# Kernel tuning notes

Measured on AMD Instinct MI355X. Metric: run time of the kernel, lower is better.

## Reference

```python
import jax, jax.numpy as jnp
import numpy as np

B, T, M, P = 512, 64, 256, 256


def setup_inputs() -> dict:
    key = jax.random.key(0)
    ks = jax.random.split(key, 17)
    w = lambda i, shape: (jax.random.normal(ks[i], shape, jnp.float32) * 0.05)
    return {
        "encoded_inputs": jax.random.normal(ks[0], (B, T, M), jnp.float32),
        "y": jax.random.normal(ks[1], (B, T, 1), jnp.float32),
        "tar": jax.random.normal(ks[2], (B, 2), jnp.float32),
        "train": 1,
        "Wd_w": w(3, (M, 2 * P)), "Wd_b": w(4, (M,)),
        "Ud_w": w(5, (M, M)),
        "vd_w": w(6, (1, M)),
        "wt_w": w(7, (1, M + 1)), "wt_b": w(8, (1,)),
        "Wy_w": w(9, (P, P + M)), "Wy_b": w(10, (P,)),
        "vy_w": w(11, (1, P)), "vy_b": w(12, (1,)),
        "Wih": w(13, (4 * P, 1)), "Whh": w(14, (4 * P, P)),
        "bih": w(15, (4 * P,)), "bhh": w(16, (4 * P,)),
    }


def _lstm_cell(x, h, c, Wih, Whh, bih, bhh):
    # torch.nn.LSTMCell gate order: i, f, g, o
    g = x @ Wih.T + h @ Whh.T + (bih + bhh)
    i, f, gg, o = jnp.split(g, 4, axis=1)
    c = jax.nn.sigmoid(f) * c + jax.nn.sigmoid(i) * jnp.tanh(gg)
    h = jax.nn.sigmoid(o) * jnp.tanh(c)
    return h, c


def reference(encoded_inputs, y, tar, train,
              Wd_w, Wd_b, Ud_w, vd_w, wt_w, wt_b,
              Wy_w, Wy_b, vy_w, vy_b, Wih, Whh, bih, bhh):
    Bn = encoded_inputs.shape[0]
    Pn = Whh.shape[1]
    Mn = encoded_inputs.shape[2]
    h0 = jnp.zeros((Bn, Pn), encoded_inputs.dtype)
    c0 = jnp.zeros((Bn, Pn), encoded_inputs.dtype)
    ctx0 = jnp.zeros((Bn, Mn), encoded_inputs.dtype)
    # U_d(encoded_inputs) is loop-invariant
    y1 = jnp.einsum('btm,nm->btn', encoded_inputs, Ud_w)  # (B,T,M)

    def attend(h, s):
        x1 = jnp.concatenate([h, s], axis=1) @ Wd_w.T + Wd_b      # (B,M)
        z1 = jnp.tanh(x1[:, None, :] + y1)                        # (B,T,M)
        l = jnp.einsum('btm,m->bt', z1, vd_w[0])                  # (B,T)
        beta = jax.nn.softmax(l, axis=1)
        return jnp.einsum('bt,btm->bm', beta, encoded_inputs)     # (B,M)

    def step(carry, y_t):
        h, s, _ = carry
        c_t = attend(h, s)
        y_til = jnp.concatenate([c_t, y_t], axis=1) @ wt_w.T + wt_b  # (B,1)
        h, s = _lstm_cell(y_til, h, s, Wih, Whh, bih, bhh)
        return (h, s, c_t), None

    (h, s, c_t), _ = jax.lax.scan(step, (h0, c0, ctx0), jnp.swapaxes(y, 0, 1))

    def head(h):
        return (jnp.concatenate([h, c_t], axis=1) @ Wy_w.T + Wy_b) @ vy_w.T + vy_b

    def extra(h, s, inp):
        y_til = jnp.concatenate([c_t, inp], axis=1) @ wt_w.T + wt_b
        h, s = _lstm_cell(y_til, h, s, Wih, Whh, bih, bhh)
        return h, s, head(h)

    y_Tp1 = head(h)
    if train:
        h, s, y_Tp2 = extra(h, s, tar[:, 0:1])
        h, s, y_Tp3 = extra(h, s, tar[:, 1:2])
    else:
        h, s, y_Tp2 = extra(h, s, y_Tp1)
        h, s, y_Tp3 = extra(h, s, y_Tp2)
    return (y_Tp1, y_Tp2, y_Tp3)
```

## Files before the change

### kernel.cpp

```cpp
#include <hip/hip_runtime.h>


typedef unsigned short u16;
typedef unsigned int u32;
typedef _Float16 half_t;
typedef half_t h2 __attribute__((ext_vector_type(2)));

#define BB 512
#define TT 64
#define MM 256
#define PP 256
#define YS 264
#define ES 68
#define NROW 2
#define NTH 1024

#define WD16_OFF  0
#define WHH16_OFF 131072
#define WY16_OFF  393216
#define WQ_ELEMS  524288
#define WQ_BYTES  (WQ_ELEMS * 2)

struct H8 { h2 p[4]; };

#if defined(__has_builtin)
#if __has_builtin(__builtin_amdgcn_fdot2)
#define FDOT2(a, b, c) __builtin_amdgcn_fdot2((a), (b), (c), false)
#endif
#endif
#ifndef FDOT2
__device__ __forceinline__ float FDOT2(h2 a, h2 b, float c) {
  return c + (float)a[0] * (float)b[0] + (float)a[1] * (float)b[1];
}
#endif

__device__ __forceinline__ float dot8(const H8 w, const H8 a, float acc) {
  acc = FDOT2(w.p[0], a.p[0], acc);
  acc = FDOT2(w.p[1], a.p[1], acc);
  acc = FDOT2(w.p[2], a.p[2], acc);
  acc = FDOT2(w.p[3], a.p[3], acc);
  return acc;
}
__device__ __forceinline__ u16 f2h(float f) {
  union { half_t h; u16 u; } x; x.h = (half_t)f; return x.u;
}
__device__ __forceinline__ float h2f(u16 u) {
  union { u16 u; half_t h; } x; x.u = u; return (float)x.h;
}
__device__ __forceinline__ void unpackH8(const H8 v, float f[8]) {
#pragma unroll
  for (int i = 0; i < 8; ++i) f[i] = (float)v.p[i >> 1][i & 1];
}
__device__ __forceinline__ void ldf8(const float* p, float f[8]) {
  float4 a = *(const float4*)p;
  float4 b = *(const float4*)(p + 4);
  f[0]=a.x; f[1]=a.y; f[2]=a.z; f[3]=a.w;
  f[4]=b.x; f[5]=b.y; f[6]=b.z; f[7]=b.w;
}
__device__ __forceinline__ float tanh_fast(float x) {
  float e = __builtin_amdgcn_exp2f(x * 2.885390081777927f);
  return 1.0f - 2.0f * __builtin_amdgcn_rcpf(1.0f + e);
}
__device__ __forceinline__ float sigmoid_fast(float x) {
  float e = __builtin_amdgcn_exp2f(x * -1.4426950408889634f);
  return __builtin_amdgcn_rcpf(1.0f + e);
}

__global__ __launch_bounds__(256) void prep_kernel(
    const float* __restrict__ Wd, const float* __restrict__ Whh,
    const float* __restrict__ Wy, u16* __restrict__ o) {
  int i = blockIdx.x * 256 + threadIdx.x;
  float v;
  if (i < WHH16_OFF) {
    int ki = i & 7, n = (i >> 3) & 255, kb = i >> 11;
    v = Wd[n * 512 + kb * 8 + ki];
  } else if (i < WY16_OFF) {
    int r = i - WHH16_OFF;
    int ki = r & 7, n = (r >> 3) & 1023, kb = r >> 13;
    v = Whh[n * 256 + kb * 8 + ki];
  } else {
    int r = i - WY16_OFF;
    int ki = r & 7, n = (r >> 3) & 255, kb = r >> 11;
    v = Wy[n * 512 + kb * 8 + ki];
  }
  o[i] = f2h(v);
}

template <int WQ>
__global__ __launch_bounds__(NTH, 4) void scan_kernel(
    const float* __restrict__ E,
    const float* __restrict__ yin,
    const float* __restrict__ tar,
    const int*   __restrict__ train,
    const void*  __restrict__ Wd_q,
    const float* __restrict__ Wd_b,
    const float* __restrict__ Ud_w,
    const float* __restrict__ vd_w,
    const float* __restrict__ wt_w,
    const float* __restrict__ wt_b,
    const void*  __restrict__ Wy_q,
    const float* __restrict__ Wy_b,
    const float* __restrict__ vy_w,
    const float* __restrict__ vy_b,
    const float* __restrict__ Wih,
    const void*  __restrict__ Whh_q,
    const float* __restrict__ bih,
    const float* __restrict__ bhh,
    float* __restrict__ out)
{
  __shared__ __align__(16) u16   y1l[NROW][TT * YS];
  __shared__ __align__(16) u16   e16T[NROW][MM * ES];
  __shared__ __align__(16) u32   hs16[NROW][256];
  __shared__ __align__(16) u32   ctx16p[NROW][128];
  __shared__ __align__(16) float px1[4][MM];
  __shared__ __align__(16) float pg[6][MM];
  __shared__ __align__(16) float pg3[4][MM];
  __shared__ __align__(16) float lpart[NROW][8][TT];
  __shared__ __align__(16) u16   betas16[NROW][TT];
  __shared__ __align__(16) float ysh[NROW][TT];
  __shared__ float red[16];
  __shared__ float sc[NROW];

  const int j   = threadIdx.x;
  const int n   = j & 255;
  const int grp = j >> 8;
  const int wv  = j >> 6;
  const int b0  = blockIdx.x * NROW;

  if (j < 512) ((u32*)hs16)[j] = 0;
  float creg0 = 0.f, creg1 = 0.f;

  const float wih0 = Wih[n],       wih1 = Wih[n + 256];
  const float wih2 = Wih[n + 512], wih3 = Wih[n + 768];
  const float bb0 = bih[n]       + bhh[n];
  const float bb1 = bih[n + 256] + bhh[n + 256];
  const float bb2 = bih[n + 512] + bhh[n + 512];
  const float bb3 = bih[n + 768] + bhh[n + 768];
  const float wtM = wt_w[MM], wtb = wt_b[0];

  if (j < NROW * TT)
    ysh[j >> 6][j & 63] = yin[(size_t)(b0 + (j >> 6)) * TT + (j & 63)];

  {
    const float* __restrict__ Eb0 = E + (size_t)b0 * TT * MM;
    for (int i = j; i < NROW * TT * MM; i += NTH) {
      int r = i >> 14;
      int idx = i & 16383;
      int t = idx >> 8, m = idx & 255;
      e16T[r][m * ES + t] = f2h(Eb0[i]);
    }
  }

  {
    const int rs = grp >> 1, ths = grp & 1;
    const float* __restrict__ Eb = E + (size_t)(b0 + rs) * TT * MM;
    const float* __restrict__ Uj = Ud_w + (size_t)n * MM;
    for (int t0 = ths * 32; t0 < ths * 32 + 32; t0 += 16) {
      float acc[16];
#pragma unroll
      for (int i = 0; i < 16; ++i) acc[i] = 0.f;
      for (int m0 = 0; m0 < MM; m0 += 8) {
        float w[8]; ldf8(Uj + m0, w);
#pragma unroll
        for (int tt = 0; tt < 16; ++tt) {
          float e[8]; ldf8(Eb + (size_t)(t0 + tt) * MM + m0, e);
#pragma unroll
          for (int mm = 0; mm < 8; ++mm) acc[tt] = fmaf(e[mm], w[mm], acc[tt]);
        }
      }
#pragma unroll
      for (int tt = 0; tt < 16; ++tt)
        y1l[rs][(t0 + tt) * YS + n] = f2h(acc[tt]);
    }
  }
  __syncthreads();

  auto gates_apply = [&](int r, float gi, float gf, float gg, float go,
                         float ytil) {
    gi += ytil * wih0 + bb0;
    gf += ytil * wih1 + bb1;
    gg += ytil * wih2 + bb2;
    go += ytil * wih3 + bb3;
    float& cr = r ? creg1 : creg0;
    float c = sigmoid_fast(gf) * cr + sigmoid_fast(gi) * tanh_fast(gg);
    float h = sigmoid_fast(go) * tanh_fast(c);
    cr = c;
    u16* hsu = (u16*)hs16[r];
    hsu[n] = f2h(h);
    hsu[256 + n] = f2h(c);
  };

  auto head_store = [&](int outIdx) {
    float p = 0.f;
    const int rr = grp >> 1, seg = grp & 1;
    const u32* st = seg ? ctx16p[rr] : hs16[rr];
    if (WQ) {
      const u16* pw = (const u16*)Wy_q + ((size_t)(seg * 32) * 256 + n) * 8;
#pragma unroll 2
      for (int kb = 0; kb < 32; ++kb) {
        H8 w = *(const H8*)pw; pw += 2048;
        H8 s = *(const H8*)&st[kb * 4];
        p = dot8(w, s, p);
      }
    } else {
      const float* W = (const float*)Wy_q + (size_t)n * 512 + seg * 256;
#pragma unroll 2
      for (int kb = 0; kb < 32; ++kb) {
        H8 sv = *(const H8*)&st[kb * 4];
        float sf[8]; unpackH8(sv, sf);
        float w[8]; ldf8(W + kb * 8, w);
#pragma unroll
        for (int i = 0; i < 8; ++i) p = fmaf(sf[i], w[i], p);
      }
    }
    if (grp) px1[grp - 1][n] = p;
    __syncthreads();
    if (grp == 0) {
      float q0 = (p + px1[0][n] + Wy_b[n]) * vy_w[n];
      float q1 = (px1[1][n] + px1[2][n] + Wy_b[n]) * vy_w[n];
#pragma unroll
      for (int off = 32; off; off >>= 1) {
        q0 += __shfl_xor(q0, off, 64);
        q1 += __shfl_xor(q1, off, 64);
      }
      if ((j & 63) == 0) { red[wv] = q0; red[8 + wv] = q1; }
    }
    __syncthreads();
    if (j == 0) {
      float o0 = red[0] + red[1] + red[2] + red[3] + vy_b[0];
      float o1 = red[8] + red[9] + red[10] + red[11] + vy_b[0];
      out[(size_t)outIdx * BB + b0] = o0;
      out[(size_t)outIdx * BB + b0 + 1] = o1;
      sc[0] = o0; sc[1] = o1;
    }
    __syncthreads();
  };

  auto mv4 = [&](float& m0, float& m1, float& m2, float& m3, float& m4,
                 float& m5) {
    m0 = m1 = m2 = m3 = m4 = m5 = 0.f;
    if (WQ) {
      const u16* Whh16 = (const u16*)Whh_q;
      if (grp < 2) {
        const int kb0 = grp << 4;
        const u16* pw = Whh16 + ((size_t)kb0 * 1024 + n) * 8;
#pragma unroll 2
        for (int kb2 = 0; kb2 < 16; ++kb2) {
          const int kb = kb0 + kb2;
          H8 h0 = *(const H8*)&hs16[0][kb * 4];
          H8 h1 = *(const H8*)&hs16[1][kb * 4];
          H8 w0 = *(const H8*)pw;
          H8 w1 = *(const H8*)(pw + 2048);
          H8 w2 = *(const H8*)(pw + 4096);
          pw += 8192;
          m0 = dot8(w0, h0, m0); m1 = dot8(w0, h1, m1);
          m2 = dot8(w1, h0, m2); m3 = dot8(w1, h1, m3);
          m4 = dot8(w2, h0, m4); m5 = dot8(w2, h1, m5);
        }
      } else {
        const int half = grp - 2;
        const u16* p3 = Whh16 + ((size_t)(half * 16) * 1024 + 768 + n) * 8;
#pragma unroll 2
        for (int kb2 = 0; kb2 < 16; ++kb2) {
          const int kg = half * 16 + kb2;
          H8 w3 = *(const H8*)p3; p3 += 8192;
          H8 h0 = *(const H8*)&hs16[0][kg * 4];
          H8 h1 = *(const H8*)&hs16[1][kg * 4];
          m0 = dot8(w3, h0, m0); m1 = dot8(w3, h1, m1);
        }
      }
    } else {
      const float* Whf = (const float*)Whh_q;
      if (grp < 2) {
        const int kb0 = grp << 4;
        const float* pw0 = Whf + (size_t)n * 256 + kb0 * 8;
        const float* pw1 = pw0 + 256 * 256;
        const float* pw2 = pw0 + 512 * 256;
#pragma unroll 2
        for (int kb2 = 0; kb2 < 16; ++kb2) {
          const int kb = kb0 + kb2;
          H8 h0v = *(const H8*)&hs16[0][kb * 4];
          H8 h1v = *(const H8*)&hs16[1][kb * 4];
          float hf0[8], hf1[8]; unpackH8(h0v, hf0); unpackH8(h1v, hf1);
          float w0[8], w1[8], w2[8];
          ldf8(pw0 + kb2 * 8, w0);
          ldf8(pw1 + kb2 * 8, w1);
          ldf8(pw2 + kb2 * 8, w2);
#pragma unroll
          for (int i = 0; i < 8; ++i) {
            m0 = fmaf(hf0[i], w0[i], m0); m1 = fmaf(hf1[i], w0[i], m1);
            m2 = fmaf(hf0[i], w1[i], m2); m3 = fmaf(hf1[i], w1[i], m3);
            m4 = fmaf(hf0[i], w2[i], m4); m5 = fmaf(hf1[i], w2[i], m5);
          }
        }
      } else {
        const int half = grp - 2;
        const float* p3f = Whf + ((size_t)(768 + n)) * 256 + half * 128;
#pragma unroll 2
        for (int kb2 = 0; kb2 < 16; ++kb2) {
          const int kg = half * 16 + kb2;
          H8 h0v = *(const H8*)&hs16[0][kg * 4];
          H8 h1v = *(const H8*)&hs16[1][kg * 4];
          float hf0[8], hf1[8]; unpackH8(h0v, hf0); unpackH8(h1v, hf1);
          float w3[8]; ldf8(p3f + kb2 * 8, w3);
#pragma unroll
          for (int i = 0; i < 8; ++i) {
            m0 = fmaf(hf0[i], w3[i], m0); m1 = fmaf(hf1[i], w3[i], m1);
          }
        }
      }
    }
  };

  for (int step = 0; step < TT; ++step) {
    float s0 = 0.f, s1 = 0.f, s2 = 0.f, s3 = 0.f, s4 = 0.f, s5 = 0.f;
    {
      float a0 = 0, a1 = 0, a2 = 0, a3 = 0, a4 = 0, a5 = 0;
      if (WQ) {
        const u16* Whh16 = (const u16*)Whh_q;
        if (grp < 2) {
          const int kb0 = grp << 4;
          const u16* pw = Whh16 + ((size_t)kb0 * 1024 + n) * 8;
#pragma unroll 2
          for (int kb2 = 0; kb2 < 16; ++kb2) {
            const int kb = kb0 + kb2;
            H8 h0 = *(const H8*)&hs16[0][kb * 4];
            H8 h1 = *(const H8*)&hs16[1][kb * 4];
            H8 w0 = *(const H8*)pw;
            H8 w1 = *(const H8*)(pw + 2048);
            H8 w2 = *(const H8*)(pw + 4096);
            pw += 8192;
            a0 = dot8(w0, h0, a0); a1 = dot8(w0, h1, a1);
            a2 = dot8(w1, h0, a2); a3 = dot8(w1, h1, a3);
            a4 = dot8(w2, h0, a4); a5 = dot8(w2, h1, a5);
          }
        } else {
          const int half = grp - 2;
          const u16* pd = (const u16*)Wd_q + ((size_t)(half * 32) * 256 + n) * 8;
          const u16* p3 = Whh16 + ((size_t)(half * 16) * 1024 + 768 + n) * 8;
#pragma unroll 2
          for (int kb2 = 0; kb2 < 16; ++kb2) {
            const int kd = half * 32 + kb2 * 2;
            const int kg = half * 16 + kb2;
            H8 s00 = *(const H8*)&hs16[0][kd * 4];
            H8 s01 = *(const H8*)&hs16[0][kd * 4 + 4];
            H8 s10 = *(const H8*)&hs16[1][kd * 4];
            H8 s11 = *(const H8*)&hs16[1][kd * 4 + 4];
            H8 wd0 = *(const H8*)pd;
            H8 wd1 = *(const H8*)(pd + 2048);
            pd += 4096;
            H8 w3 = *(const H8*)p3; p3 += 8192;
            H8 h0 = *(const H8*)&hs16[0][kg * 4];
            H8 h1 = *(const H8*)&hs16[1][kg * 4];
            a0 = dot8(wd0, s00, a0); a0 = dot8(wd1, s01, a0);
            a1 = dot8(wd0, s10, a1); a1 = dot8(wd1, s11, a1);
            a2 = dot8(w3, h0, a2);   a3 = dot8(w3, h1, a3);
          }
        }
      } else {
        const float* Whf = (const float*)Whh_q;
        if (grp < 2) {
          const int kb0 = grp << 4;
          const float* pw0 = Whf + (size_t)n * 256 + kb0 * 8;
          const float* pw1 = pw0 + 256 * 256;
          const float* pw2 = pw0 + 512 * 256;
#pragma unroll 2
          for (int kb2 = 0; kb2 < 16; ++kb2) {
            const int kb = kb0 + kb2;
            H8 h0v = *(const H8*)&hs16[0][kb * 4];
            H8 h1v = *(const H8*)&hs16[1][kb * 4];
            float hf0[8], hf1[8]; unpackH8(h0v, hf0); unpackH8(h1v, hf1);
            float w0[8], w1[8], w2[8];
            ldf8(pw0 + kb2 * 8, w0);
            ldf8(pw1 + kb2 * 8, w1);
            ldf8(pw2 + kb2 * 8, w2);
#pragma unroll
            for (int i = 0; i < 8; ++i) {
              a0 = fmaf(hf0[i], w0[i], a0); a1 = fmaf(hf1[i], w0[i], a1);
              a2 = fmaf(hf0[i], w1[i], a2); a3 = fmaf(hf1[i], w1[i], a3);
              a4 = fmaf(hf0[i], w2[i], a4); a5 = fmaf(hf1[i], w2[i], a5);
            }
          }
        } else {
          const int half = grp - 2;
          const float* Wdf = (const float*)Wd_q + (size_t)n * 512 + half * 256;
          const float* p3f = Whf + ((size_t)(768 + n)) * 256 + half * 128;
#pragma unroll 2
          for (int kb2 = 0; kb2 < 16; ++kb2) {
            const int kd = half * 32 + kb2 * 2;
            const int kg = half * 16 + kb2;
            H8 s00v = *(const H8*)&hs16[0][kd * 4];
            H8 s01v = *(const H8*)&hs16[0][kd * 4 + 4];
            H8 s10v = *(const H8*)&hs16[1][kd * 4];
            H8 s11v = *(const H8*)&hs16[1][kd * 4 + 4];
            float f00[8], f01[8], f10[8], f11[8];
            unpackH8(s00v, f00); unpackH8(s01v, f01);
            unpackH8(s10v, f10); unpackH8(s11v, f11);
            H8 h0v = *(const H8*)&hs16[0][kg * 4];
            H8 h1v = *(const H8*)&hs16[1][kg * 4];
            float hf0[8], hf1[8]; unpackH8(h0v, hf0); unpackH8(h1v, hf1);
            float wd0[8], wd1[8], w3[8];
            ldf8(Wdf + kb2 * 16, wd0);
            ldf8(Wdf + kb2 * 16 + 8, wd1);
            ldf8(p3f + kb2 * 8, w3);
#pragma unroll
            for (int i = 0; i < 8; ++i) {
              a0 = fmaf(f00[i], wd0[i], a0); a0 = fmaf(f01[i], wd1[i], a0);
              a1 = fmaf(f10[i], wd0[i], a1); a1 = fmaf(f11[i], wd1[i], a1);
              a2 = fmaf(hf0[i], w3[i], a2);  a3 = fmaf(hf1[i], w3[i], a3);
            }
          }
        }
      }
      if (grp == 0) {
        s0 = a0; s1 = a1; s2 = a2; s3 = a3; s4 = a4; s5 = a5;
      } else if (grp == 1) {
        pg[0][n] = a0; pg[1][n] = a1; pg[2][n] = a2;
        pg[3][n] = a3; pg[4][n] = a4; pg[5][n] = a5;
      } else if (grp == 2) {
        float bia = Wd_b[n];
        px1[0][n] = a0 + bia; px1[1][n] = a1 + bia;
        pg3[0][n] = a2; pg3[1][n] = a3;
      } else {
        px1[2][n] = a0; px1[3][n] = a1;
        pg3[2][n] = a2; pg3[3][n] = a3;
      }
    }
    __syncthreads();

    {
      const int r = j >> 9, e8 = (j >> 6) & 7, t = j & 63;
      const u16* __restrict__ yrow = &y1l[r][t * YS + e8 * 32];
      const float* __restrict__ xh = &px1[r][e8 * 32];
      const float* __restrict__ xc = &px1[2 + r][e8 * 32];
      const float* __restrict__ vp = vd_w + e8 * 32;
      float lp = 0.f;
#pragma unroll
      for (int m0 = 0; m0 < 32; m0 += 8) {
        H8 yv = *(const H8*)(yrow + m0);
        float yf[8]; unpackH8(yv, yf);
        float xf[8]; ldf8(xh + m0, xf);
        float xg[8]; ldf8(xc + m0, xg);
        float vf[8]; ldf8(vp + m0, vf);
#pragma unroll
        for (int mm = 0; mm < 8; ++mm) {
          float z = tanh_fast(xf[mm] + xg[mm] + yf[mm]);
          lp = fmaf(z, vf[mm], lp);
        }
      }
      lpart[r][e8][t] = lp;
    }
    __syncthreads();

    if ((j & 511) < 64) {
      const int r = j >> 9, t = j & 63;
      float l = lpart[r][0][t] + lpart[r][1][t] + lpart[r][2][t] +
                lpart[r][3][t] + lpart[r][4][t] + lpart[r][5][t] +
                lpart[r][6][t] + lpart[r][7][t];
      float mx = l;
#pragma unroll
      for (int off = 32; off; off >>= 1) mx = fmaxf(mx, __shfl_xor(mx, off, 64));
      float e = __builtin_amdgcn_exp2f((l - mx) * 1.4426950408889634f);
      float sm = e;
#pragma unroll
      for (int off = 32; off; off >>= 1) sm += __shfl_xor(sm, off, 64);
      betas16[r][t] = f2h(e * __builtin_amdgcn_rcpf(sm));
    }
    __syncthreads();

    if (((j >> 8) & 1) == 0) {
      const int r = j >> 9;
      const u16* __restrict__ ep = &e16T[r][n * ES];
      float acc = 0.f;
#pragma unroll
      for (int t0 = 0; t0 < TT; t0 += 8) {
        h2 e0 = *(const h2*)(ep + t0);
        h2 e1 = *(const h2*)(ep + t0 + 2);
        h2 e2 = *(const h2*)(ep + t0 + 4);
        h2 e3 = *(const h2*)(ep + t0 + 6);
        H8 bp = *(const H8*)&betas16[r][t0];
        acc = FDOT2(bp.p[0], e0, acc);
        acc = FDOT2(bp.p[1], e1, acc);
        acc = FDOT2(bp.p[2], e2, acc);
        acc = FDOT2(bp.p[3], e3, acc);
      }
      ((u16*)ctx16p[r])[n] = f2h(acc);
      float p = acc * wt_w[n];
#pragma unroll
      for (int off = 32; off; off >>= 1) p += __shfl_xor(p, off, 64);
      if ((j & 63) == 0) red[wv] = p;
    }
    __syncthreads();

    if (grp == 0) {
      float yt0 = red[0] + red[1] + red[2] + red[3] + ysh[0][step] * wtM + wtb;
      float yt1 = red[8] + red[9] + red[10] + red[11] + ysh[1][step] * wtM + wtb;
      gates_apply(0, s0 + pg[0][n], s2 + pg[2][n], s4 + pg[4][n],
                  pg3[0][n] + pg3[2][n], yt0);
      gates_apply(1, s1 + pg[1][n], s3 + pg[3][n], s5 + pg[5][n],
                  pg3[1][n] + pg3[3][n], yt1);
    }
    __syncthreads();
  }

  if (((j >> 8) & 1) == 0) {
    const int r = j >> 9;
    float p = h2f(((const u16*)ctx16p[r])[n]) * wt_w[n];
#pragma unroll
    for (int off = 32; off; off >>= 1) p += __shfl_xor(p, off, 64);
    if ((j & 63) == 0) red[wv] = p;
  }
  __syncthreads();
  const float ctd0 = red[0] + red[1] + red[2] + red[3];
  const float ctd1 = red[8] + red[9] + red[10] + red[11];

  head_store(0);

  const int tr = train[0];
  for (int e = 0; e < 2; ++e) {
    float m0, m1, m2, m3, m4, m5;
    mv4(m0, m1, m2, m3, m4, m5);
    if (grp == 1) {
      pg[0][n] = m0; pg[1][n] = m1; pg[2][n] = m2;
      pg[3][n] = m3; pg[4][n] = m4; pg[5][n] = m5;
    } else if (grp == 2) {
      pg3[0][n] = m0; pg3[1][n] = m1;
    } else if (grp == 3) {
      pg3[2][n] = m0; pg3[3][n] = m1;
    }
    __syncthreads();
    if (grp == 0) {
      float inp0 = tr ? tar[(size_t)b0 * 2 + e] : sc[0];
      float inp1 = tr ? tar[(size_t)(b0 + 1) * 2 + e] : sc[1];
      float yt0 = ctd0 + inp0 * wtM + wtb;
      float yt1 = ctd1 + inp1 * wtM + wtb;
      gates_apply(0, m0 + pg[0][n], m2 + pg[2][n], m4 + pg[4][n],
                  pg3[0][n] + pg3[2][n], yt0);
      gates_apply(1, m1 + pg[1][n], m3 + pg[3][n], m5 + pg[5][n],
                  pg3[1][n] + pg3[3][n], yt1);
    }
    __syncthreads();
    head_store(1 + e);
  }
}

extern "C" void kernel_launch(void* const* d_in, const int* in_sizes, int n_in,
                              void* d_out, int out_size, void* d_ws, size_t ws_size,
                              hipStream_t stream) {
  const float* E     = (const float*)d_in[0];
  const float* yin   = (const float*)d_in[1];
  const float* tar   = (const float*)d_in[2];
  const int*   train = (const int*)d_in[3];
  const float* Wd_w  = (const float*)d_in[4];
  const float* Wd_b  = (const float*)d_in[5];
  const float* Ud_w  = (const float*)d_in[6];
  const float* vd_w  = (const float*)d_in[7];
  const float* wt_w  = (const float*)d_in[8];
  const float* wt_b  = (const float*)d_in[9];
  const float* Wy_w  = (const float*)d_in[10];
  const float* Wy_b  = (const float*)d_in[11];
  const float* vy_w  = (const float*)d_in[12];
  const float* vy_b  = (const float*)d_in[13];
  const float* Wih   = (const float*)d_in[14];
  const float* Whh   = (const float*)d_in[15];
  const float* bih   = (const float*)d_in[16];
  const float* bhh   = (const float*)d_in[17];

  float* out = (float*)d_out;

  if (ws_size >= (size_t)WQ_BYTES) {
    u16* wq = (u16*)d_ws;
    prep_kernel<<<dim3(WQ_ELEMS / 256), dim3(256), 0, stream>>>(
        Wd_w, Whh, Wy_w, wq);
    scan_kernel<1><<<dim3(BB / NROW), dim3(NTH), 0, stream>>>(
        E, yin, tar, train, wq + WD16_OFF, Wd_b, Ud_w, vd_w, wt_w, wt_b,
        wq + WY16_OFF, Wy_b, vy_w, vy_b, Wih, wq + WHH16_OFF, bih, bhh, out);
  } else {
    scan_kernel<0><<<dim3(BB / NROW), dim3(NTH), 0, stream>>>(
        E, yin, tar, train, Wd_w, Wd_b, Ud_w, vd_w, wt_w, wt_b,
        Wy_w, Wy_b, vy_w, vy_b, Wih, Whh, bih, bhh, out);
  }

  (void)in_sizes; (void)n_in; (void)out_size;
}
```

Before: 1.087 ms.

## Rebalance per-step matvecs evenly across all four thread groups with contiguous weight layout

Repacks the fp16 Wd and Whh weights so each of the 1024 threads reads one contiguous 384-element slice. Every thread now computes an equal share: a quarter-K slice of the Wd projection plus two Whh gate partial sums. This replaces the old scheme where groups did unequal work with strided weight reads. Gate partials are stored as fp16 in shared memory and summed by the gate threads. The softmax and context stages are merged to drop one barrier, and the head matvec gives two rows to each of 512 threads. The fp16 rounding of gate partials adds precision risk, and the tanh input now sums four partial vectors.

```diff
diff --git a/kernel.cpp b/kernel.cpp
--- a/kernel.cpp
+++ b/kernel.cpp
@@ -9,14 +9,11 @@
 #define BB 512
 #define TT 64
 #define MM 256
-#define PP 256
 #define YS 264
 #define ES 68
 #define NROW 2
 #define NTH 1024
 
-#define WD16_OFF  0
-#define WHH16_OFF 131072
 #define WY16_OFF  393216
 #define WQ_ELEMS  524288
 #define WQ_BYTES  (WQ_ELEMS * 2)
@@ -69,21 +66,25 @@
 __global__ __launch_bounds__(256) void prep_kernel(
     const float* __restrict__ Wd, const float* __restrict__ Whh,
     const float* __restrict__ Wy, u16* __restrict__ o) {
-  int i = blockIdx.x * 256 + threadIdx.x;
+  int u = blockIdx.x * 256 + threadIdx.x;
   float v;
-  if (i < WHH16_OFF) {
-    int ki = i & 7, n = (i >> 3) & 255, kb = i >> 11;
-    v = Wd[n * 512 + kb * 8 + ki];
-  } else if (i < WY16_OFF) {
-    int r = i - WHH16_OFF;
-    int ki = r & 7, n = (r >> 3) & 1023, kb = r >> 13;
-    v = Whh[n * 256 + kb * 8 + ki];
+  if (u < WY16_OFF) {
+    int c = u / 384, s = u % 384;
+    int q = c >> 8, n = c & 255;
+    int part = s >> 7, rem = s & 127;
+    if (part == 0) {
+      v = Wd[n * 512 + q * 128 + rem];
+    } else {
+      int g = 2 * (q >> 1) + (part - 1);
+      v = Whh[(n + 256 * g) * 256 + (q & 1) * 128 + rem];
+    }
   } else {
-    int r = i - WY16_OFF;
-    int ki = r & 7, n = (r >> 3) & 255, kb = r >> 11;
-    v = Wy[n * 512 + kb * 8 + ki];
-  }
-  o[i] = f2h(v);
+    int w = u - WY16_OFF;
+    int c = w >> 8, rem = w & 255;
+    int kh = c >> 8, n = c & 255;
+    v = Wy[n * 512 + kh * 256 + rem];
+  }
+  o[u] = f2h(v);
 }
 
 template <int WQ>
@@ -112,18 +113,17 @@
   __shared__ __align__(16) u16   e16T[NROW][MM * ES];
   __shared__ __align__(16) u32   hs16[NROW][256];
   __shared__ __align__(16) u32   ctx16p[NROW][128];
-  __shared__ __align__(16) float px1[4][MM];
-  __shared__ __align__(16) float pg[6][MM];
-  __shared__ __align__(16) float pg3[4][MM];
+  __shared__ __align__(16) float px1[8 * MM];
+  __shared__ __align__(16) u16   pgs[16 * MM];
   __shared__ __align__(16) float lpart[NROW][8][TT];
-  __shared__ __align__(16) u16   betas16[NROW][TT];
+  __shared__ __align__(16) u16   betas16[8][TT];
   __shared__ __align__(16) float ysh[NROW][TT];
   __shared__ float red[16];
   __shared__ float sc[NROW];
 
   const int j   = threadIdx.x;
   const int n   = j & 255;
-  const int grp = j >> 8;
+  const int q   = j >> 8;
   const int wv  = j >> 6;
   const int b0  = blockIdx.x * NROW;
 
@@ -152,7 +152,7 @@
   }
 
   {
-    const int rs = grp >> 1, ths = grp & 1;
+    const int rs = q >> 1, ths = q & 1;
     const float* __restrict__ Eb = E + (size_t)(b0 + rs) * TT * MM;
     const float* __restrict__ Uj = Ud_w + (size_t)n * MM;
     for (int t0 = ths * 32; t0 < ths * 32 + 32; t0 += 16) {
@@ -190,45 +190,62 @@
     hsu[256 + n] = f2h(c);
   };
 
+  auto gate_combine = [&](int r, float& gi, float& gf, float& gg, float& go) {
+    gi = h2f(pgs[(0 * 2 + r) * 256 + n]) + h2f(pgs[(2 * 2 + r) * 256 + n]);
+    gf = h2f(pgs[(1 * 2 + r) * 256 + n]) + h2f(pgs[(3 * 2 + r) * 256 + n]);
+    gg = h2f(pgs[(4 * 2 + r) * 256 + n]) + h2f(pgs[(6 * 2 + r) * 256 + n]);
+    go = h2f(pgs[(5 * 2 + r) * 256 + n]) + h2f(pgs[(7 * 2 + r) * 256 + n]);
+  };
+
   auto head_store = [&](int outIdx) {
-    float p = 0.f;
-    const int rr = grp >> 1, seg = grp & 1;
-    const u32* st = seg ? ctx16p[rr] : hs16[rr];
-    if (WQ) {
-      const u16* pw = (const u16*)Wy_q + ((size_t)(seg * 32) * 256 + n) * 8;
+    if (j < 512) {
+      const int kh = j >> 8, nn = j & 255;
+      float p0 = 0.f, p1 = 0.f;
+      const u32* s0 = kh ? ctx16p[0] : hs16[0];
+      const u32* s1 = kh ? ctx16p[1] : hs16[1];
+      if (WQ) {
+        const u16* pw = (const u16*)Wy_q + ((size_t)(kh * 256 + nn)) * 256;
+#pragma unroll 4
+        for (int i = 0; i < 32; ++i) {
+          H8 w = *(const H8*)(pw + i * 8);
+          H8 a0 = *(const H8*)&s0[i * 4];
+          H8 a1 = *(const H8*)&s1[i * 4];
+          p0 = dot8(w, a0, p0);
+          p1 = dot8(w, a1, p1);
+        }
+      } else {
+        const float* W = (const float*)Wy_q + (size_t)nn * 512 + kh * 256;
 #pragma unroll 2
-      for (int kb = 0; kb < 32; ++kb) {
-        H8 w = *(const H8*)pw; pw += 2048;
-        H8 s = *(const H8*)&st[kb * 4];
-        p = dot8(w, s, p);
-      }
-    } else {
-      const float* W = (const float*)Wy_q + (size_t)n * 512 + seg * 256;
-#pragma unroll 2
-      for (int kb = 0; kb < 32; ++kb) {
-        H8 sv = *(const H8*)&st[kb * 4];
-        float sf[8]; unpackH8(sv, sf);
-        float w[8]; ldf8(W + kb * 8, w);
-#pragma unroll
-        for (int i = 0; i < 8; ++i) p = fmaf(sf[i], w[i], p);
-      }
-    }
-    if (grp) px1[grp - 1][n] = p;
-    __syncthreads();
-    if (grp == 0) {
-      float q0 = (p + px1[0][n] + Wy_b[n]) * vy_w[n];
-      float q1 = (px1[1][n] + px1[2][n] + Wy_b[n]) * vy_w[n];
+        for (int i = 0; i < 32; ++i) {
+          H8 a0v = *(const H8*)&s0[i * 4];
+          H8 a1v = *(const H8*)&s1[i * 4];
+          float a0[8], a1[8]; unpackH8(a0v, a0); unpackH8(a1v, a1);
+          float w[8]; ldf8(W + i * 8, w);
+#pragma unroll
+          for (int m = 0; m < 8; ++m) {
+            p0 = fmaf(a0[m], w[m], p0);
+            p1 = fmaf(a1[m], w[m], p1);
+          }
+        }
+      }
+      px1[(kh * 2 + 0) * 256 + nn] = p0;
+      px1[(kh * 2 + 1) * 256 + nn] = p1;
+    }
+    __syncthreads();
+    if (j < 256) {
+      float q0 = (px1[n] + px1[2 * 256 + n] + Wy_b[n]) * vy_w[n];
+      float q1 = (px1[1 * 256 + n] + px1[3 * 256 + n] + Wy_b[n]) * vy_w[n];
 #pragma unroll
       for (int off = 32; off; off >>= 1) {
         q0 += __shfl_xor(q0, off, 64);
         q1 += __shfl_xor(q1, off, 64);
       }
-      if ((j & 63) == 0) { red[wv] = q0; red[8 + wv] = q1; }
+      if ((j & 63) == 0) { red[wv] = q0; red[4 + wv] = q1; }
     }
     __syncthreads();
     if (j == 0) {
       float o0 = red[0] + red[1] + red[2] + red[3] + vy_b[0];
-      float o1 = red[8] + red[9] + red[10] + red[11] + vy_b[0];
+      float o1 = red[4] + red[5] + red[6] + red[7] + vy_b[0];
       out[(size_t)outIdx * BB + b0] = o0;
       out[(size_t)outIdx * BB + b0 + 1] = o1;
       sc[0] = o0; sc[1] = o1;
@@ -236,215 +253,85 @@
     __syncthreads();
   };
 
-  auto mv4 = [&](float& m0, float& m1, float& m2, float& m3, float& m4,
-                 float& m5) {
-    m0 = m1 = m2 = m3 = m4 = m5 = 0.f;
-    if (WQ) {
-      const u16* Whh16 = (const u16*)Whh_q;
-      if (grp < 2) {
-        const int kb0 = grp << 4;
-        const u16* pw = Whh16 + ((size_t)kb0 * 1024 + n) * 8;
+  const int cw = q * 64;
+  const int gw = (q & 1) * 64;
+
+  for (int step = 0; step < TT; ++step) {
+    {
+      float ax0 = 0.f, ax1 = 0.f;
+      float ga0 = 0.f, ga1 = 0.f, gb0 = 0.f, gb1 = 0.f;
+      if (WQ) {
+        const u16* base = (const u16*)Wd_q + (size_t)j * 384;
+        const u32* h0p = hs16[0];
+        const u32* h1p = hs16[1];
+#pragma unroll 4
+        for (int i = 0; i < 16; ++i) {
+          H8 wd = *(const H8*)(base + i * 8);
+          H8 wa = *(const H8*)(base + 128 + i * 8);
+          H8 wb = *(const H8*)(base + 256 + i * 8);
+          H8 cs0 = *(const H8*)&h0p[cw + i * 4];
+          H8 cs1 = *(const H8*)&h1p[cw + i * 4];
+          H8 hh0 = *(const H8*)&h0p[gw + i * 4];
+          H8 hh1 = *(const H8*)&h1p[gw + i * 4];
+          ax0 = dot8(wd, cs0, ax0); ax1 = dot8(wd, cs1, ax1);
+          ga0 = dot8(wa, hh0, ga0); ga1 = dot8(wa, hh1, ga1);
+          gb0 = dot8(wb, hh0, gb0); gb1 = dot8(wb, hh1, gb1);
+        }
+      } else {
+        const int gsel = 2 * (q >> 1);
+        const float* pwd = (const float*)Wd_q + (size_t)n * 512 + q * 128;
+        const float* pwa = (const float*)Whh_q +
+                           ((size_t)(n + 256 * gsel)) * 256 + (q & 1) * 128;
+        const float* pwb = pwa + 256 * 256;
 #pragma unroll 2
-        for (int kb2 = 0; kb2 < 16; ++kb2) {
-          const int kb = kb0 + kb2;
-          H8 h0 = *(const H8*)&hs16[0][kb * 4];
-          H8 h1 = *(const H8*)&hs16[1][kb * 4];
-          H8 w0 = *(const H8*)pw;
-          H8 w1 = *(const H8*)(pw + 2048);
-          H8 w2 = *(const H8*)(pw + 4096);
-          pw += 8192;
-          m0 = dot8(w0, h0, m0); m1 = dot8(w0, h1, m1);
-          m2 = dot8(w1, h0, m2); m3 = dot8(w1, h1, m3);
-          m4 = dot8(w2, h0, m4); m5 = dot8(w2, h1, m5);
-        }
-      } else {
-        const int half = grp - 2;
-        const u16* p3 = Whh16 + ((size_t)(half * 16) * 1024 + 768 + n) * 8;
-#pragma unroll 2
-        for (int kb2 = 0; kb2 < 16; ++kb2) {
-          const int kg = half * 16 + kb2;
-          H8 w3 = *(const H8*)p3; p3 += 8192;
-          H8 h0 = *(const H8*)&hs16[0][kg * 4];
-          H8 h1 = *(const H8*)&hs16[1][kg * 4];
-          m0 = dot8(w3, h0, m0); m1 = dot8(w3, h1, m1);
-        }
-      }
-    } else {
-      const float* Whf = (const float*)Whh_q;
-      if (grp < 2) {
-        const int kb0 = grp << 4;
-        const float* pw0 = Whf + (size_t)n * 256 + kb0 * 8;
-        const float* pw1 = pw0 + 256 * 256;
-        const float* pw2 = pw0 + 512 * 256;
-#pragma unroll 2
-        for (int kb2 = 0; kb2 < 16; ++kb2) {
-          const int kb = kb0 + kb2;
-          H8 h0v = *(const H8*)&hs16[0][kb * 4];
-          H8 h1v = *(const H8*)&hs16[1][kb * 4];
-          float hf0[8], hf1[8]; unpackH8(h0v, hf0); unpackH8(h1v, hf1);
-          float w0[8], w1[8], w2[8];
-          ldf8(pw0 + kb2 * 8, w0);
-          ldf8(pw1 + kb2 * 8, w1);
-          ldf8(pw2 + kb2 * 8, w2);
-#pragma unroll
-          for (int i = 0; i < 8; ++i) {
-            m0 = fmaf(hf0[i], w0[i], m0); m1 = fmaf(hf1[i], w0[i], m1);
-            m2 = fmaf(hf0[i], w1[i], m2); m3 = fmaf(hf1[i], w1[i], m3);
-            m4 = fmaf(hf0[i], w2[i], m4); m5 = fmaf(hf1[i], w2[i], m5);
+        for (int i = 0; i < 16; ++i) {
+          H8 cs0v = *(const H8*)&hs16[0][cw + i * 4];
+          H8 cs1v = *(const H8*)&hs16[1][cw + i * 4];
+          H8 hh0v = *(const H8*)&hs16[0][gw + i * 4];
+          H8 hh1v = *(const H8*)&hs16[1][gw + i * 4];
+          float c0[8], c1[8], h0f[8], h1f[8];
+          unpackH8(cs0v, c0); unpackH8(cs1v, c1);
+          unpackH8(hh0v, h0f); unpackH8(hh1v, h1f);
+          float wd8[8], wa8[8], wb8[8];
+          ldf8(pwd + i * 8, wd8); ldf8(pwa + i * 8, wa8); ldf8(pwb + i * 8, wb8);
+#pragma unroll
+          for (int m = 0; m < 8; ++m) {
+            ax0 = fmaf(c0[m], wd8[m], ax0); ax1 = fmaf(c1[m], wd8[m], ax1);
+            ga0 = fmaf(h0f[m], wa8[m], ga0); ga1 = fmaf(h1f[m], wa8[m], ga1);
+            gb0 = fmaf(h0f[m], wb8[m], gb0); gb1 = fmaf(h1f[m], wb8[m], gb1);
           }
         }
-      } else {
-        const int half = grp - 2;
-        const float* p3f = Whf + ((size_t)(768 + n)) * 256 + half * 128;
-#pragma unroll 2
-        for (int kb2 = 0; kb2 < 16; ++kb2) {
-          const int kg = half * 16 + kb2;
-          H8 h0v = *(const H8*)&hs16[0][kg * 4];
-          H8 h1v = *(const H8*)&hs16[1][kg * 4];
-          float hf0[8], hf1[8]; unpackH8(h0v, hf0); unpackH8(h1v, hf1);
-          float w3[8]; ldf8(p3f + kb2 * 8, w3);
-#pragma unroll
-          for (int i = 0; i < 8; ++i) {
-            m0 = fmaf(hf0[i], w3[i], m0); m1 = fmaf(hf1[i], w3[i], m1);
-          }
-        }
-      }
-    }
-  };
-
-  for (int step = 0; step < TT; ++step) {
-    float s0 = 0.f, s1 = 0.f, s2 = 0.f, s3 = 0.f, s4 = 0.f, s5 = 0.f;
-    {
-      float a0 = 0, a1 = 0, a2 = 0, a3 = 0, a4 = 0, a5 = 0;
-      if (WQ) {
-        const u16* Whh16 = (const u16*)Whh_q;
-        if (grp < 2) {
-          const int kb0 = grp << 4;
-          const u16* pw = Whh16 + ((size_t)kb0 * 1024 + n) * 8;
-#pragma unroll 2
-          for (int kb2 = 0; kb2 < 16; ++kb2) {
-            const int kb = kb0 + kb2;
-            H8 h0 = *(const H8*)&hs16[0][kb * 4];
-            H8 h1 = *(const H8*)&hs16[1][kb * 4];
-            H8 w0 = *(const H8*)pw;
-            H8 w1 = *(const H8*)(pw + 2048);
-            H8 w2 = *(const H8*)(pw + 4096);
-            pw += 8192;
-            a0 = dot8(w0, h0, a0); a1 = dot8(w0, h1, a1);
-            a2 = dot8(w1, h0, a2); a3 = dot8(w1, h1, a3);
-            a4 = dot8(w2, h0, a4); a5 = dot8(w2, h1, a5);
-          }
-        } else {
-          const int half = grp - 2;
-          const u16* pd = (const u16*)Wd_q + ((size_t)(half * 32) * 256 + n) * 8;
-          const u16* p3 = Whh16 + ((size_t)(half * 16) * 1024 + 768 + n) * 8;
-#pragma unroll 2
-          for (int kb2 = 0; kb2 < 16; ++kb2) {
-            const int kd = half * 32 + kb2 * 2;
-            const int kg = half * 16 + kb2;
-            H8 s00 = *(const H8*)&hs16[0][kd * 4];
-            H8 s01 = *(const H8*)&hs16[0][kd * 4 + 4];
-            H8 s10 = *(const H8*)&hs16[1][kd * 4];
-            H8 s11 = *(const H8*)&hs16[1][kd * 4 + 4];
-            H8 wd0 = *(const H8*)pd;
-            H8 wd1 = *(const H8*)(pd + 2048);
-            pd += 4096;
-            H8 w3 = *(const H8*)p3; p3 += 8192;
-            H8 h0 = *(const H8*)&hs16[0][kg * 4];
-            H8 h1 = *(const H8*)&hs16[1][kg * 4];
-            a0 = dot8(wd0, s00, a0); a0 = dot8(wd1, s01, a0);
-            a1 = dot8(wd0, s10, a1); a1 = dot8(wd1, s11, a1);
-            a2 = dot8(w3, h0, a2);   a3 = dot8(w3, h1, a3);
-          }
-        }
-      } else {
-        const float* Whf = (const float*)Whh_q;
-        if (grp < 2) {
-          const int kb0 = grp << 4;
-          const float* pw0 = Whf + (size_t)n * 256 + kb0 * 8;
-          const float* pw1 = pw0 + 256 * 256;
-          const float* pw2 = pw0 + 512 * 256;
-#pragma unroll 2
-          for (int kb2 = 0; kb2 < 16; ++kb2) {
-            const int kb = kb0 + kb2;
-            H8 h0v = *(const H8*)&hs16[0][kb * 4];
-            H8 h1v = *(const H8*)&hs16[1][kb * 4];
-            float hf0[8], hf1[8]; unpackH8(h0v, hf0); unpackH8(h1v, hf1);
-            float w0[8], w1[8], w2[8];
-            ldf8(pw0 + kb2 * 8, w0);
-            ldf8(pw1 + kb2 * 8, w1);
-            ldf8(pw2 + kb2 * 8, w2);
-#pragma unroll
-            for (int i = 0; i < 8; ++i) {
-              a0 = fmaf(hf0[i], w0[i], a0); a1 = fmaf(hf1[i], w0[i], a1);
-              a2 = fmaf(hf0[i], w1[i], a2); a3 = fmaf(hf1[i], w1[i], a3);
-              a4 = fmaf(hf0[i], w2[i], a4); a5 = fmaf(hf1[i], w2[i], a5);
-            }
-          }
-        } else {
-          const int half = grp - 2;
-          const float* Wdf = (const float*)Wd_q + (size_t)n * 512 + half * 256;
-          const float* p3f = Whf + ((size_t)(768 + n)) * 256 + half * 128;
-#pragma unroll 2
-          for (int kb2 = 0; kb2 < 16; ++kb2) {
-            const int kd = half * 32 + kb2 * 2;
-            const int kg = half * 16 + kb2;
-            H8 s00v = *(const H8*)&hs16[0][kd * 4];
-            H8 s01v = *(const H8*)&hs16[0][kd * 4 + 4];
-            H8 s10v = *(const H8*)&hs16[1][kd * 4];
-            H8 s11v = *(const H8*)&hs16[1][kd * 4 + 4];
-            float f00[8], f01[8], f10[8], f11[8];
-            unpackH8(s00v, f00); unpackH8(s01v, f01);
-            unpackH8(s10v, f10); unpackH8(s11v, f11);
-            H8 h0v = *(const H8*)&hs16[0][kg * 4];
-            H8 h1v = *(const H8*)&hs16[1][kg * 4];
-            float hf0[8], hf1[8]; unpackH8(h0v, hf0); unpackH8(h1v, hf1);
-            float wd0[8], wd1[8], w3[8];
-            ldf8(Wdf + kb2 * 16, wd0);
-            ldf8(Wdf + kb2 * 16 + 8, wd1);
-            ldf8(p3f + kb2 * 8, w3);
-#pragma unroll
-            for (int i = 0; i < 8; ++i) {
-              a0 = fmaf(f00[i], wd0[i], a0); a0 = fmaf(f01[i], wd1[i], a0);
-              a1 = fmaf(f10[i], wd0[i], a1); a1 = fmaf(f11[i], wd1[i], a1);
-              a2 = fmaf(hf0[i], w3[i], a2);  a3 = fmaf(hf1[i], w3[i], a3);
-            }
-          }
-        }
-      }
-      if (grp == 0) {
-        s0 = a0; s1 = a1; s2 = a2; s3 = a3; s4 = a4; s5 = a5;
-      } else if (grp == 1) {
-        pg[0][n] = a0; pg[1][n] = a1; pg[2][n] = a2;
-        pg[3][n] = a3; pg[4][n] = a4; pg[5][n] = a5;
-      } else if (grp == 2) {
-        float bia = Wd_b[n];
-        px1[0][n] = a0 + bia; px1[1][n] = a1 + bia;
-        pg3[0][n] = a2; pg3[1][n] = a3;
-      } else {
-        px1[2][n] = a0; px1[3][n] = a1;
-        pg3[2][n] = a2; pg3[3][n] = a3;
-      }
+      }
+      if (q == 0) { float b = Wd_b[n]; ax0 += b; ax1 += b; }
+      px1[(0 * 4 + q) * 256 + n] = ax0;
+      px1[(1 * 4 + q) * 256 + n] = ax1;
+      pgs[((q * 2 + 0) * 2 + 0) * 256 + n] = f2h(ga0);
+      pgs[((q * 2 + 0) * 2 + 1) * 256 + n] = f2h(ga1);
+      pgs[((q * 2 + 1) * 2 + 0) * 256 + n] = f2h(gb0);
+      pgs[((q * 2 + 1) * 2 + 1) * 256 + n] = f2h(gb1);
     }
     __syncthreads();
 
     {
       const int r = j >> 9, e8 = (j >> 6) & 7, t = j & 63;
-      const u16* __restrict__ yrow = &y1l[r][t * YS + e8 * 32];
-      const float* __restrict__ xh = &px1[r][e8 * 32];
-      const float* __restrict__ xc = &px1[2 + r][e8 * 32];
-      const float* __restrict__ vp = vd_w + e8 * 32;
+      const int mb = e8 * 32;
+      const u16* __restrict__ yrow = &y1l[r][t * YS + mb];
+      const float* p0 = &px1[(r * 4 + 0) * 256 + mb];
+      const float* p1 = &px1[(r * 4 + 1) * 256 + mb];
+      const float* p2 = &px1[(r * 4 + 2) * 256 + mb];
+      const float* p3 = &px1[(r * 4 + 3) * 256 + mb];
+      const float* vp = vd_w + mb;
       float lp = 0.f;
 #pragma unroll
       for (int m0 = 0; m0 < 32; m0 += 8) {
-        H8 yv = *(const H8*)(yrow + m0);
-        float yf[8]; unpackH8(yv, yf);
-        float xf[8]; ldf8(xh + m0, xf);
-        float xg[8]; ldf8(xc + m0, xg);
-        float vf[8]; ldf8(vp + m0, vf);
+        float xa[8], xb[8], xc[8], xd[8], vf[8], yf[8];
+        ldf8(p0 + m0, xa); ldf8(p1 + m0, xb);
+        ldf8(p2 + m0, xc); ldf8(p3 + m0, xd);
+        H8 yv = *(const H8*)(yrow + m0); unpackH8(yv, yf);
+        ldf8(vp + m0, vf);
 #pragma unroll
         for (int mm = 0; mm < 8; ++mm) {
-          float z = tanh_fast(xf[mm] + xg[mm] + yf[mm]);
+          float z = tanh_fast(xa[mm] + xb[mm] + xc[mm] + xd[mm] + yf[mm]);
           lp = fmaf(z, vf[mm], lp);
         }
       }
@@ -452,11 +339,11 @@
     }
     __syncthreads();
 
-    if ((j & 511) < 64) {
-      const int r = j >> 9, t = j & 63;
-      float l = lpart[r][0][t] + lpart[r][1][t] + lpart[r][2][t] +
-                lpart[r][3][t] + lpart[r][4][t] + lpart[r][5][t] +
-                lpart[r][6][t] + lpart[r][7][t];
+    if (j < 512) {
+      const int r = j >> 8, lane = j & 63;
+      float l = lpart[r][0][lane] + lpart[r][1][lane] + lpart[r][2][lane] +
+                lpart[r][3][lane] + lpart[r][4][lane] + lpart[r][5][lane] +
+                lpart[r][6][lane] + lpart[r][7][lane];
       float mx = l;
 #pragma unroll
       for (int off = 32; off; off >>= 1) mx = fmaxf(mx, __shfl_xor(mx, off, 64));
@@ -464,25 +351,22 @@
       float sm = e;
 #pragma unroll
       for (int off = 32; off; off >>= 1) sm += __shfl_xor(sm, off, 64);
-      betas16[r][t] = f2h(e * __builtin_amdgcn_rcpf(sm));
-    }
-    __syncthreads();
-
-    if (((j >> 8) & 1) == 0) {
-      const int r = j >> 9;
+      betas16[wv][lane] = f2h(e * __builtin_amdgcn_rcpf(sm));
+      asm volatile("s_waitcnt lgkmcnt(0)" ::: "memory");
+      const u16* __restrict__ bp = betas16[wv];
       const u16* __restrict__ ep = &e16T[r][n * ES];
       float acc = 0.f;
 #pragma unroll
       for (int t0 = 0; t0 < TT; t0 += 8) {
+        H8 bv = *(const H8*)(bp + t0);
         h2 e0 = *(const h2*)(ep + t0);
         h2 e1 = *(const h2*)(ep + t0 + 2);
         h2 e2 = *(const h2*)(ep + t0 + 4);
         h2 e3 = *(const h2*)(ep + t0 + 6);
-        H8 bp = *(const H8*)&betas16[r][t0];
-        acc = FDOT2(bp.p[0], e0, acc);
-        acc = FDOT2(bp.p[1], e1, acc);
-        acc = FDOT2(bp.p[2], e2, acc);
-        acc = FDOT2(bp.p[3], e3, acc);
+        acc = FDOT2(bv.p[0], e0, acc);
+        acc = FDOT2(bv.p[1], e1, acc);
+        acc = FDOT2(bv.p[2], e2, acc);
+        acc = FDOT2(bv.p[3], e3, acc);
       }
       ((u16*)ctx16p[r])[n] = f2h(acc);
       float p = acc * wt_w[n];
@@ -492,19 +376,20 @@
     }
     __syncthreads();
 
-    if (grp == 0) {
+    if (j < 256) {
       float yt0 = red[0] + red[1] + red[2] + red[3] + ysh[0][step] * wtM + wtb;
-      float yt1 = red[8] + red[9] + red[10] + red[11] + ysh[1][step] * wtM + wtb;
-      gates_apply(0, s0 + pg[0][n], s2 + pg[2][n], s4 + pg[4][n],
-                  pg3[0][n] + pg3[2][n], yt0);
-      gates_apply(1, s1 + pg[1][n], s3 + pg[3][n], s5 + pg[5][n],
-                  pg3[1][n] + pg3[3][n], yt1);
-    }
-    __syncthreads();
-  }
-
-  if (((j >> 8) & 1) == 0) {
-    const int r = j >> 9;
+      float yt1 = red[4] + red[5] + red[6] + red[7] + ysh[1][step] * wtM + wtb;
+      float gi, gf, gg, go;
+      gate_combine(0, gi, gf, gg, go);
+      gates_apply(0, gi, gf, gg, go, yt0);
+      gate_combine(1, gi, gf, gg, go);
+      gates_apply(1, gi, gf, gg, go, yt1);
+    }
+    __syncthreads();
+  }
+
+  if (j < 512) {
+    const int r = j >> 8;
     float p = h2f(((const u16*)ctx16p[r])[n]) * wt_w[n];
 #pragma unroll
     for (int off = 32; off; off >>= 1) p += __shfl_xor(p, off, 64);
@@ -512,32 +397,62 @@
   }
   __syncthreads();
   const float ctd0 = red[0] + red[1] + red[2] + red[3];
-  const float ctd1 = red[8] + red[9] + red[10] + red[11];
+  const float ctd1 = red[4] + red[5] + red[6] + red[7];
 
   head_store(0);
 
   const int tr = train[0];
   for (int e = 0; e < 2; ++e) {
-    float m0, m1, m2, m3, m4, m5;
-    mv4(m0, m1, m2, m3, m4, m5);
-    if (grp == 1) {
-      pg[0][n] = m0; pg[1][n] = m1; pg[2][n] = m2;
-      pg[3][n] = m3; pg[4][n] = m4; pg[5][n] = m5;
-    } else if (grp == 2) {
-      pg3[0][n] = m0; pg3[1][n] = m1;
-    } else if (grp == 3) {
-      pg3[2][n] = m0; pg3[3][n] = m1;
-    }
-    __syncthreads();
-    if (grp == 0) {
+    {
+      float ga0 = 0.f, ga1 = 0.f, gb0 = 0.f, gb1 = 0.f;
+      if (WQ) {
+        const u16* base = (const u16*)Wd_q + (size_t)j * 384;
+        const u32* h0p = hs16[0];
+        const u32* h1p = hs16[1];
+#pragma unroll 4
+        for (int i = 0; i < 16; ++i) {
+          H8 wa = *(const H8*)(base + 128 + i * 8);
+          H8 wb = *(const H8*)(base + 256 + i * 8);
+          H8 hh0 = *(const H8*)&h0p[gw + i * 4];
+          H8 hh1 = *(const H8*)&h1p[gw + i * 4];
+          ga0 = dot8(wa, hh0, ga0); ga1 = dot8(wa, hh1, ga1);
+          gb0 = dot8(wb, hh0, gb0); gb1 = dot8(wb, hh1, gb1);
+        }
+      } else {
+        const int gsel = 2 * (q >> 1);
+        const float* pwa = (const float*)Whh_q +
+                           ((size_t)(n + 256 * gsel)) * 256 + (q & 1) * 128;
+        const float* pwb = pwa + 256 * 256;
+#pragma unroll 2
+        for (int i = 0; i < 16; ++i) {
+          H8 hh0v = *(const H8*)&hs16[0][gw + i * 4];
+          H8 hh1v = *(const H8*)&hs16[1][gw + i * 4];
+          float h0f[8], h1f[8]; unpackH8(hh0v, h0f); unpackH8(hh1v, h1f);
+          float wa8[8], wb8[8];
+          ldf8(pwa + i * 8, wa8); ldf8(pwb + i * 8, wb8);
+#pragma unroll
+          for (int m = 0; m < 8; ++m) {
+            ga0 = fmaf(h0f[m], wa8[m], ga0); ga1 = fmaf(h1f[m], wa8[m], ga1);
+            gb0 = fmaf(h0f[m], wb8[m], gb0); gb1 = fmaf(h1f[m], wb8[m], gb1);
+          }
+        }
+      }
+      pgs[((q * 2 + 0) * 2 + 0) * 256 + n] = f2h(ga0);
+      pgs[((q * 2 + 0) * 2 + 1) * 256 + n] = f2h(ga1);
+      pgs[((q * 2 + 1) * 2 + 0) * 256 + n] = f2h(gb0);
+      pgs[((q * 2 + 1) * 2 + 1) * 256 + n] = f2h(gb1);
+    }
+    __syncthreads();
+    if (j < 256) {
       float inp0 = tr ? tar[(size_t)b0 * 2 + e] : sc[0];
       float inp1 = tr ? tar[(size_t)(b0 + 1) * 2 + e] : sc[1];
       float yt0 = ctd0 + inp0 * wtM + wtb;
       float yt1 = ctd1 + inp1 * wtM + wtb;
-      gates_apply(0, m0 + pg[0][n], m2 + pg[2][n], m4 + pg[4][n],
-                  pg3[0][n] + pg3[2][n], yt0);
-      gates_apply(1, m1 + pg[1][n], m3 + pg[3][n], m5 + pg[5][n],
-                  pg3[1][n] + pg3[3][n], yt1);
+      float gi, gf, gg, go;
+      gate_combine(0, gi, gf, gg, go);
+      gates_apply(0, gi, gf, gg, go, yt0);
+      gate_combine(1, gi, gf, gg, go);
+      gates_apply(1, gi, gf, gg, go, yt1);
     }
     __syncthreads();
     head_store(1 + e);
@@ -573,8 +488,8 @@
     prep_kernel<<<dim3(WQ_ELEMS / 256), dim3(256), 0, stream>>>(
         Wd_w, Whh, Wy_w, wq);
     scan_kernel<1><<<dim3(BB / NROW), dim3(NTH), 0, stream>>>(
-        E, yin, tar, train, wq + WD16_OFF, Wd_b, Ud_w, vd_w, wt_w, wt_b,
-        wq + WY16_OFF, Wy_b, vy_w, vy_b, Wih, wq + WHH16_OFF, bih, bhh, out);
+        E, yin, tar, train, wq, Wd_b, Ud_w, vd_w, wt_w, wt_b,
+        wq + WY16_OFF, Wy_b, vy_w, vy_b, Wih, wq, bih, bhh, out);
   } else {
     scan_kernel<0><<<dim3(BB / NROW), dim3(NTH), 0, stream>>>(
         E, yin, tar, train, Wd_w, Wd_b, Ud_w, vd_w, wt_w, wt_b,
```

New measurement: 3.590 ms. 3.3x slower.
